# Kernel optimization log

Hardware: AMD Instinct MI355X
Metric: run time of the kernel (lower is better)

Reference implementation:

```python
import jax, jax.numpy as jnp
import numpy as np

B, F, S, D, H = 32, 4096, 8, 512, 2048
N_ITERS = 3
EPS = 1e-8
SCALE = D ** -0.5
LN_EPS = 1e-5  # torch LayerNorm default


def setup_inputs() -> dict:
    key = jax.random.key(0)
    ks = jax.random.split(key, 16)
    w = lambda k, shp: (jax.random.normal(k, shp) * 0.02).astype(jnp.float32)
    d = {
        "slots": jax.random.normal(ks[0], (B, S, D), dtype=jnp.float32),
        "features": jax.random.normal(ks[1], (B, F, D), dtype=jnp.float32),
        # projection weights, stored (in, out) so y = x @ W
        "w_k": w(ks[2], (D, D)),
        "w_v": w(ks[3], (D, D)),
        "w_q": w(ks[4], (D, D)),
        # layer norms
        "ln_feat_w": jnp.ones(D, jnp.float32), "ln_feat_b": jnp.zeros(D, jnp.float32),
        "ln_slot_w": jnp.ones(D, jnp.float32), "ln_slot_b": jnp.zeros(D, jnp.float32),
        # GRUCell (torch layout: gates [r, z, n] stacked on dim0 of [3D, D])
        "gru_w_ih": w(ks[5], (3 * D, D)),
        "gru_w_hh": w(ks[6], (3 * D, D)),
        "gru_b_ih": jnp.zeros(3 * D, jnp.float32),
        "gru_b_hh": jnp.zeros(3 * D, jnp.float32),
        # residual MLP: LN -> Linear(D,H) -> relu -> Linear(H,D)
        "ln_mlp_w": jnp.ones(D, jnp.float32), "ln_mlp_b": jnp.zeros(D, jnp.float32),
        "mlp_w1": w(ks[7], (D, H)), "mlp_b1": jnp.zeros(H, jnp.float32),
        "mlp_w2": w(ks[8], (H, D)), "mlp_b2": jnp.zeros(D, jnp.float32),
    }
    return d


def _ln(x, w, b):
    m = jnp.mean(x, axis=-1, keepdims=True)
    v = jnp.mean(jnp.square(x - m), axis=-1, keepdims=True)
    return (x - m) * jax.lax.rsqrt(v + LN_EPS) * w + b


def _gru_cell(x, h, w_ih, w_hh, b_ih, b_hh):
    # torch.nn.GRUCell semantics; x,h: [..., D]
    gi = x @ w_ih.T + b_ih
    gh = h @ w_hh.T + b_hh
    i_r, i_z, i_n = jnp.split(gi, 3, axis=-1)
    h_r, h_z, h_n = jnp.split(gh, 3, axis=-1)
    r = jax.nn.sigmoid(i_r + h_r)
    z = jax.nn.sigmoid(i_z + h_z)
    n = jnp.tanh(i_n + r * h_n)
    return (1.0 - z) * n + z * h


def reference(slots, features, w_k, w_v, w_q, ln_feat_w, ln_feat_b,
              ln_slot_w, ln_slot_b, gru_w_ih, gru_w_hh, gru_b_ih, gru_b_hh,
              ln_mlp_w, ln_mlp_b, mlp_w1, mlp_b1, mlp_w2, mlp_b2):
    f = _ln(features, ln_feat_w, ln_feat_b)          # [B,F,D]
    keys = f @ w_k                                    # [B,F,D]
    values = f @ w_v                                  # [B,F,D]
    pre_norm_attn = None
    for _ in range(N_ITERS):
        s_n = _ln(slots, ln_slot_w, ln_slot_b)        # [B,S,D]
        q = s_n @ w_q                                 # [B,S,D]
        dots = jnp.einsum('bsd,bfd->bsf', q, keys) * SCALE
        pre_norm_attn = jax.nn.softmax(dots, axis=1)  # softmax over SLOTS
        attn = pre_norm_attn + EPS
        attn = attn / jnp.sum(attn, axis=-1, keepdims=True)
        updates = jnp.einsum('bsf,bfd->bsd', attn, values)
        slots = _gru_cell(updates, s_n, gru_w_ih, gru_w_hh, gru_b_ih, gru_b_hh)
        # residual MLP with initial LayerNorm
        h = _ln(slots, ln_mlp_w, ln_mlp_b)
        h = jax.nn.relu(h @ mlp_w1 + mlp_b1) @ mlp_w2 + mlp_b2
        slots = slots + h
    return slots, pre_norm_attn
```

## Files before the change

kernel.cpp:

```cpp
#include <hip/hip_runtime.h>
#include <hip/hip_bf16.h>
#include <stdint.h>

typedef __hip_bfloat16 bf16;
typedef unsigned short ushort_t;

#define B_ 32
#define F_ 4096
#define S_ 8
#define D_ 512
#define H_ 2048
#define LN_EPS 1e-5f
#define EPS_ 1e-8f
#define SCALE_ 0.044194173824159216f

__device__ __forceinline__ float b2f(ushort_t u){
  union { uint32_t i; float f; } c; c.i = ((uint32_t)u) << 16; return c.f;
}
__device__ __forceinline__ float4 ld4f(const float* p){ return *(const float4*)p; }
__device__ __forceinline__ float4 ld4h(const ushort_t* p){
  ushort4 u = *(const ushort4*)p;
  return make_float4(b2f(u.x), b2f(u.y), b2f(u.z), b2f(u.w));
}
__device__ __forceinline__ float allsum64(float v){
  #pragma unroll
  for (int o = 1; o < 64; o <<= 1) v += __shfl_xor(v, o, 64);
  return v;
}
__device__ __forceinline__ float blockSum256(float v, float* sh){
  v = allsum64(v);
  int wid = threadIdx.x >> 6, lane = threadIdx.x & 63;
  __syncthreads();
  if (lane == 0) sh[wid] = v;
  __syncthreads();
  return sh[0] + sh[1] + sh[2] + sh[3];
}

__global__ void detect_dtype(const uint32_t* __restrict__ w, int* __restrict__ flag){
  __shared__ int sh;
  if (threadIdx.x == 0) sh = 0;
  __syncthreads();
  int c = 0;
  for (int i = threadIdx.x; i < 4096; i += 256){
    uint32_t e = (w[i] >> 7) & 0xFF;
    if (e == 0 || e >= 0xBF) c++;
  }
  atomicAdd(&sh, c);
  __syncthreads();
  if (threadIdx.x == 0) *flag = (sh >= 100) ? 1 : 0;
}

template<int TRANS_B, int BIAS, int RELU, int A_DYN, int B_DYN>
__global__ __launch_bounds__(256) void gemm64(
    const void* __restrict__ A, const void* __restrict__ B,
    const void* __restrict__ bias, float* __restrict__ C,
    int M, int N, int K, int kLen, const int* __restrict__ flag)
{
  const bool f32 = (*flag != 0);
  const bool aF = A_DYN ? f32 : true;
  const bool bF = B_DYN ? f32 : true;
  __shared__ float As[16][68];
  __shared__ float Bs[16][68];
  const int tid = threadIdx.x;
  const int m0 = blockIdx.x * 64, n0 = blockIdx.y * 64;
  const int kBeg = blockIdx.z * kLen;
  const int tm = (tid & 15) * 4, tn = (tid >> 4) * 4;
  const int ar = tid >> 2;
  const int ac = (tid & 3) * 4;
  const int br = tid >> 4;
  const int bc = (tid & 15) * 4;
  float acc[4][4] = {};

  for (int kc = kBeg; kc < kBeg + kLen; kc += 16){
    size_t aidx = (size_t)(m0 + ar) * K + kc + ac;
    float4 a4 = aF ? ld4f((const float*)A + aidx) : ld4h((const ushort_t*)A + aidx);
    As[ac+0][ar] = a4.x; As[ac+1][ar] = a4.y; As[ac+2][ar] = a4.z; As[ac+3][ar] = a4.w;
    if (!TRANS_B){
      size_t bidx = (size_t)(kc + br) * N + n0 + bc;
      float4 b4 = bF ? ld4f((const float*)B + bidx) : ld4h((const ushort_t*)B + bidx);
      Bs[br][bc+0] = b4.x; Bs[br][bc+1] = b4.y; Bs[br][bc+2] = b4.z; Bs[br][bc+3] = b4.w;
    } else {
      size_t bidx = (size_t)(n0 + ar) * K + kc + ac;
      float4 b4 = bF ? ld4f((const float*)B + bidx) : ld4h((const ushort_t*)B + bidx);
      Bs[ac+0][ar] = b4.x; Bs[ac+1][ar] = b4.y; Bs[ac+2][ar] = b4.z; Bs[ac+3][ar] = b4.w;
    }
    __syncthreads();
    #pragma unroll
    for (int k = 0; k < 16; k++){
      float av[4], bv[4];
      #pragma unroll
      for (int i = 0; i < 4; i++) av[i] = As[k][tm + i];
      #pragma unroll
      for (int j = 0; j < 4; j++) bv[j] = Bs[k][tn + j];
      #pragma unroll
      for (int i = 0; i < 4; i++)
        #pragma unroll
        for (int j = 0; j < 4; j++) acc[i][j] += av[i] * bv[j];
    }
    __syncthreads();
  }
  float bb[4] = {0,0,0,0};
  if (BIAS){
    #pragma unroll
    for (int j = 0; j < 4; j++)
      bb[j] = f32 ? ((const float*)bias)[n0 + tn + j]
                  : b2f(((const ushort_t*)bias)[n0 + tn + j]);
  }
  #pragma unroll
  for (int i = 0; i < 4; i++){
    #pragma unroll
    for (int j = 0; j < 4; j++){
      float v = acc[i][j];
      if (BIAS) v += bb[j];
      if (RELU) v = fmaxf(v, 0.0f);
      C[((size_t)blockIdx.z * M + m0 + tm + i) * N + n0 + tn + j] = v;
    }
  }
}

template<int BIAS, int RELU>
__global__ __launch_bounds__(256) void combine4(
    const float* __restrict__ in, const void* __restrict__ bias,
    float* __restrict__ out, int sz, int N)
{
  int i = blockIdx.x * 256 + threadIdx.x;
  float v = in[i] + in[sz + i] + in[2 * sz + i] + in[3 * sz + i];
  if (BIAS) v += b2f(((const ushort_t*)bias)[i % N]);
  if (RELU) v = fmaxf(v, 0.0f);
  out[i] = v;
}

template<int F32>
__global__ __launch_bounds__(256, 2) void big_pass(
    const void* __restrict__ features, const float* __restrict__ qk,
    const void* __restrict__ lnw, const void* __restrict__ lnb,
    void* __restrict__ d_out_base, float* __restrict__ Upart,
    float* __restrict__ Rpart, const int* __restrict__ flag)
{
  if ((*flag != 0) != (F32 != 0)) return;
  __shared__ float Ubuf[4][S_ * D_];
  __shared__ float Rbuf[4][S_];
  __shared__ float pbuf[S_][256];
  const int b = blockIdx.y;
  const int tid = threadIdx.x;
  const int wid = tid >> 6, lane = tid & 63;
  const int fblock = blockIdx.x * 256;
  const int f0 = fblock + wid * 64;

  float lw[8], lb[8];
  #pragma unroll
  for (int j = 0; j < 8; j++){
    int d = 8 * lane + j;
    lw[j] = F32 ? ((const float*)lnw)[d] : b2f(((const ushort_t*)lnw)[d]);
    lb[j] = F32 ? ((const float*)lnb)[d] : b2f(((const ushort_t*)lnb)[d]);
  }
  float qkr[8][8];
  #pragma unroll
  for (int s = 0; s < 8; s++){
    const float* qp = qk + (size_t)(b * S_ + s) * D_ + 8 * lane;
    float4 q0 = *(const float4*)qp;
    float4 q1 = *(const float4*)(qp + 4);
    qkr[s][0]=q0.x; qkr[s][1]=q0.y; qkr[s][2]=q0.z; qkr[s][3]=q0.w;
    qkr[s][4]=q1.x; qkr[s][5]=q1.y; qkr[s][6]=q1.z; qkr[s][7]=q1.w;
  }
  float U[8][8];
  #pragma unroll
  for (int s = 0; s < 8; s++)
    #pragma unroll
    for (int j = 0; j < 8; j++) U[s][j] = 0.0f;
  float racc[8] = {0,0,0,0,0,0,0,0};

  const size_t base = ((size_t)b * F_ + f0) * D_ + 8 * lane;
  const float* fbf = (const float*)features + base;
  const ushort_t* fbh = (const ushort_t*)features + base;
  float4 nf0 = {}, nf1 = {}; uint4 nh = {};
  if (F32){ nf0 = *(const float4*)fbf; nf1 = *(const float4*)(fbf + 4); }
  else    { nh  = *(const uint4*)fbh; }

  for (int r = 0; r < 64; r++){
    float x[8];
    if (F32){
      float4 c0 = nf0, c1 = nf1;
      if (r < 63){
        nf0 = *(const float4*)(fbf + (size_t)(r + 1) * D_);
        nf1 = *(const float4*)(fbf + (size_t)(r + 1) * D_ + 4);
      }
      x[0]=c0.x; x[1]=c0.y; x[2]=c0.z; x[3]=c0.w;
      x[4]=c1.x; x[5]=c1.y; x[6]=c1.z; x[7]=c1.w;
    } else {
      uint4 cx = nh;
      if (r < 63) nh = *(const uint4*)(fbh + (size_t)(r + 1) * D_);
      x[0]=b2f(cx.x & 0xffff); x[1]=b2f(cx.x >> 16);
      x[2]=b2f(cx.y & 0xffff); x[3]=b2f(cx.y >> 16);
      x[4]=b2f(cx.z & 0xffff); x[5]=b2f(cx.z >> 16);
      x[6]=b2f(cx.w & 0xffff); x[7]=b2f(cx.w >> 16);
    }
    float sum = 0.0f;
    #pragma unroll
    for (int j = 0; j < 8; j++) sum += x[j];
    float mean = allsum64(sum) * (1.0f / 512.0f);
    float var = 0.0f;
    #pragma unroll
    for (int j = 0; j < 8; j++){ x[j] -= mean; var += x[j] * x[j]; }
    var = allsum64(var) * (1.0f / 512.0f);
    float rstd = 1.0f / sqrtf(var + LN_EPS);
    float y[8];
    #pragma unroll
    for (int j = 0; j < 8; j++) y[j] = x[j] * rstd * lw[j] + lb[j];

    float dt[8];
    #pragma unroll
    for (int s = 0; s < 8; s++){
      float t = 0.0f;
      #pragma unroll
      for (int j = 0; j < 8; j++) t += qkr[s][j] * y[j];
      dt[s] = allsum64(t) * SCALE_;
    }
    float mx = dt[0];
    #pragma unroll
    for (int s = 1; s < 8; s++) mx = fmaxf(mx, dt[s]);
    float p[8]; float den = 0.0f;
    #pragma unroll
    for (int s = 0; s < 8; s++){ p[s] = __expf(dt[s] - mx); den += p[s]; }
    float inv = 1.0f / den;
    #pragma unroll
    for (int s = 0; s < 8; s++) p[s] *= inv;
    #pragma unroll
    for (int s = 0; s < 8; s++) if (lane == s) pbuf[s][wid * 64 + r] = p[s];
    #pragma unroll
    for (int s = 0; s < 8; s++){
      float pe = p[s] + EPS_;
      racc[s] += pe;
      #pragma unroll
      for (int j = 0; j < 8; j++) U[s][j] += pe * y[j];
    }
  }
  #pragma unroll
  for (int s = 0; s < 8; s++){
    float* ub = &Ubuf[wid][s * D_ + 8 * lane];
    *(float4*)ub     = make_float4(U[s][0], U[s][1], U[s][2], U[s][3]);
    *(float4*)(ub+4) = make_float4(U[s][4], U[s][5], U[s][6], U[s][7]);
  }
  #pragma unroll
  for (int s = 0; s < 8; s++) if (lane == s) Rbuf[wid][s] = racc[s];
  __syncthreads();
  float* up = Upart + (size_t)(b * 16 + blockIdx.x) * S_ * D_;
  for (int e = tid; e < S_ * D_; e += 256)
    up[e] = Ubuf[0][e] + Ubuf[1][e] + Ubuf[2][e] + Ubuf[3][e];
  if (tid < 8)
    Rpart[(b * 16 + blockIdx.x) * S_ + tid] =
        Rbuf[0][tid] + Rbuf[1][tid] + Rbuf[2][tid] + Rbuf[3][tid];
  #pragma unroll
  for (int s = 0; s < 8; s++){
    size_t oi = 131072 + ((size_t)(b * S_ + s)) * F_ + fblock + tid;
    float pv = pbuf[s][tid];
    if (F32) ((float*)d_out_base)[oi] = pv;
    else     ((bf16*)d_out_base)[oi] = __float2bfloat16(pv);
  }
}

__global__ __launch_bounds__(256) void reduce_updates(
    const float* __restrict__ Upart, const float* __restrict__ Rpart,
    float* __restrict__ Ud)
{
  __shared__ float rinv;
  int bs = blockIdx.x;
  int b = bs >> 3, s = bs & 7;
  int t = threadIdx.x;
  if (t == 0){
    float r = 0.0f;
    for (int w = 0; w < 16; w++) r += Rpart[(b * 16 + w) * S_ + s];
    rinv = 1.0f / r;
  }
  __syncthreads();
  const float* up = Upart + ((size_t)(b * 16) * S_ + s) * D_;
  float ri = rinv;
  #pragma unroll
  for (int u = 0; u < 2; u++){
    int e = t + u * 256;
    float acc = 0.0f;
    for (int w = 0; w < 16; w++) acc += up[(size_t)w * S_ * D_ + e];
    Ud[((size_t)(b * S_ + s)) * D_ + e] = acc * ri;
  }
}

__global__ __launch_bounds__(256) void ln_rows(
    const float* __restrict__ x, const void* __restrict__ w,
    const void* __restrict__ b, float* __restrict__ y, const int* __restrict__ flag)
{
  const bool f32 = (*flag != 0);
  __shared__ float sh[4];
  int row = blockIdx.x, t = threadIdx.x;
  const float* xr = x + (size_t)row * D_;
  float v0 = xr[t], v1 = xr[t + 256];
  float mean = blockSum256(v0 + v1, sh) * (1.0f / 512.0f);
  float d0 = v0 - mean, d1 = v1 - mean;
  float var = blockSum256(d0 * d0 + d1 * d1, sh) * (1.0f / 512.0f);
  float rstd = 1.0f / sqrtf(var + LN_EPS);
  float w0 = f32 ? ((const float*)w)[t]       : b2f(((const ushort_t*)w)[t]);
  float w1 = f32 ? ((const float*)w)[t + 256] : b2f(((const ushort_t*)w)[t + 256]);
  float b0 = f32 ? ((const float*)b)[t]       : b2f(((const ushort_t*)b)[t]);
  float b1 = f32 ? ((const float*)b)[t + 256] : b2f(((const ushort_t*)b)[t + 256]);
  y[(size_t)row * D_ + t]       = d0 * rstd * w0 + b0;
  y[(size_t)row * D_ + t + 256] = d1 * rstd * w1 + b1;
}

__global__ __launch_bounds__(256) void gru_gate_ln(
    const float* __restrict__ gi, const float* __restrict__ gh,
    const float* __restrict__ sn, const void* __restrict__ lw,
    const void* __restrict__ lb, float* __restrict__ snew,
    float* __restrict__ lnm, const int* __restrict__ flag)
{
  const bool f32 = (*flag != 0);
  __shared__ float sh[4];
  int row = blockIdx.x, t = threadIdx.x;
  const float* gir = gi + (size_t)row * 1536;
  const float* ghr = gh + (size_t)row * 1536;
  const float* snr = sn + (size_t)row * D_;
  float v[2];
  #pragma unroll
  for (int u = 0; u < 2; u++){
    int d = t + u * 256;
    float ir = gir[d], iz = gir[512 + d], in_ = gir[1024 + d];
    float hr = ghr[d], hz = ghr[512 + d], hn = ghr[1024 + d];
    float rg = 1.0f / (1.0f + __expf(-(ir + hr)));
    float zg = 1.0f / (1.0f + __expf(-(iz + hz)));
    float a  = in_ + rg * hn;
    float e2 = __expf(2.0f * a);
    float ng = 1.0f - 2.0f / (e2 + 1.0f);
    float h  = snr[d];
    v[u] = (1.0f - zg) * ng + zg * h;
    snew[(size_t)row * D_ + d] = v[u];
  }
  float mean = blockSum256(v[0] + v[1], sh) * (1.0f / 512.0f);
  float d0 = v[0] - mean, d1 = v[1] - mean;
  float var = blockSum256(d0 * d0 + d1 * d1, sh) * (1.0f / 512.0f);
  float rstd = 1.0f / sqrtf(var + LN_EPS);
  float w0 = f32 ? ((const float*)lw)[t]       : b2f(((const ushort_t*)lw)[t]);
  float w1 = f32 ? ((const float*)lw)[t + 256] : b2f(((const ushort_t*)lw)[t + 256]);
  float b0 = f32 ? ((const float*)lb)[t]       : b2f(((const ushort_t*)lb)[t]);
  float b1 = f32 ? ((const float*)lb)[t + 256] : b2f(((const ushort_t*)lb)[t + 256]);
  lnm[(size_t)row * D_ + t]       = d0 * rstd * w0 + b0;
  lnm[(size_t)row * D_ + t + 256] = d1 * rstd * w1 + b1;
}

__global__ __launch_bounds__(256) void combine_h2(
    const float* __restrict__ snew, const float* __restrict__ h2p,
    const void* __restrict__ b2, float* __restrict__ slots,
    const int* __restrict__ flag)
{
  const bool f32 = (*flag != 0);
  int idx = blockIdx.x * 256 + threadIdx.x;
  int d = idx & 511;
  float bias = f32 ? ((const float*)b2)[d] : b2f(((const ushort_t*)b2)[d]);
  slots[idx] = snew[idx] + h2p[idx] + h2p[131072 + idx] + h2p[262144 + idx]
             + h2p[393216 + idx] + bias;
}

__global__ __launch_bounds__(256) void cast_in(const void* __restrict__ in,
                                               float* __restrict__ out,
                                               const int* __restrict__ flag){
  const bool f32 = (*flag != 0);
  int i = blockIdx.x * 256 + threadIdx.x;
  out[i] = f32 ? ((const float*)in)[i] : b2f(((const ushort_t*)in)[i]);
}
__global__ __launch_bounds__(256) void store_out(const float* __restrict__ in,
                                                 void* __restrict__ out,
                                                 const int* __restrict__ flag){
  const bool f32 = (*flag != 0);
  int i = blockIdx.x * 256 + threadIdx.x;
  float v = in[i];
  if (f32) ((float*)out)[i] = v;
  else     ((bf16*)out)[i] = __float2bfloat16(v);
}

extern "C" void kernel_launch(void* const* d_in, const int* in_sizes, int n_in,
                              void* d_out, int out_size, void* d_ws, size_t ws_size,
                              hipStream_t stream)
{
  const void* in_slots  = d_in[0];
  const void* features  = d_in[1];
  const void* w_k   = d_in[2];
  const void* w_v   = d_in[3];
  const void* w_q   = d_in[4];
  const void* ln_feat_w = d_in[5];
  const void* ln_feat_b = d_in[6];
  const void* ln_slot_w = d_in[7];
  const void* ln_slot_b = d_in[8];
  const void* w_ih  = d_in[9];
  const void* w_hh  = d_in[10];
  const void* b_ih  = d_in[11];
  const void* b_hh  = d_in[12];
  const void* ln_mlp_w = d_in[13];
  const void* ln_mlp_b = d_in[14];
  const void* mlp_w1 = d_in[15];
  const void* mlp_b1 = d_in[16];
  const void* mlp_w2 = d_in[17];
  const void* mlp_b2 = d_in[18];

  float* W     = (float*)d_ws;
  int*   flag  = (int*)d_ws;
  float* Wqk   = W + 64;
  float* slots = Wqk + 262144;
  float* s_n   = slots + 131072;
  float* qkb   = s_n + 131072;
  float* Ud    = qkb + 131072;
  float* upd   = Ud + 131072;
  float* Rpart = upd + 131072;
  float* P     = Rpart + 4096;
  float* Upart = P;
  float* gi    = P;
  float* gh    = P + 393216;
  float* lnm   = P + 786432;
  float* snew  = P + 917504;
  float* h1    = P + 1048576;
  float* h2p   = P + 1572864;
  float* Wqkp  = P + 2097152;
  float* qkp   = Wqkp + 1048576;
  float* updp  = qkp + 524288;
  float* gip   = updp + 524288;
  float* ghp   = gip + 1572864;
  float* h1p   = ghp + 1572864;

  detect_dtype<<<1, 256, 0, stream>>>((const uint32_t*)features, flag);
  cast_in<<<512, 256, 0, stream>>>(in_slots, slots, flag);
  gemm64<1, 0, 0, 1, 1><<<dim3(8, 8, 4), 256, 0, stream>>>(
      w_q, w_k, nullptr, Wqkp, 512, 512, 512, 128, flag);
  combine4<0, 0><<<1024, 256, 0, stream>>>(Wqkp, nullptr, Wqk, 262144, 512);

  for (int it = 0; it < 3; ++it){
    ln_rows<<<256, 256, 0, stream>>>(slots, ln_slot_w, ln_slot_b, s_n, flag);
    gemm64<0, 0, 0, 0, 0><<<dim3(4, 8, 4), 256, 0, stream>>>(
        s_n, Wqk, nullptr, qkp, 256, 512, 512, 128, flag);
    combine4<0, 0><<<512, 256, 0, stream>>>(qkp, nullptr, qkb, 131072, 512);
    big_pass<0><<<dim3(16, 32), 256, 0, stream>>>(
        features, qkb, ln_feat_w, ln_feat_b, d_out, Upart, Rpart, flag);
    big_pass<1><<<dim3(16, 32), 256, 0, stream>>>(
        features, qkb, ln_feat_w, ln_feat_b, d_out, Upart, Rpart, flag);
    reduce_updates<<<256, 256, 0, stream>>>(Upart, Rpart, Ud);
    gemm64<0, 0, 0, 0, 1><<<dim3(4, 8, 4), 256, 0, stream>>>(
        Ud, w_v, nullptr, updp, 256, 512, 512, 128, flag);
    combine4<0, 0><<<512, 256, 0, stream>>>(updp, nullptr, upd, 131072, 512);
    gemm64<1, 0, 0, 0, 1><<<dim3(4, 24, 4), 256, 0, stream>>>(
        upd, w_ih, nullptr, gip, 256, 1536, 512, 128, flag);
    combine4<1, 0><<<1536, 256, 0, stream>>>(gip, b_ih, gi, 393216, 1536);
    gemm64<1, 0, 0, 0, 1><<<dim3(4, 24, 4), 256, 0, stream>>>(
        s_n, w_hh, nullptr, ghp, 256, 1536, 512, 128, flag);
    combine4<1, 0><<<1536, 256, 0, stream>>>(ghp, b_hh, gh, 393216, 1536);
    gru_gate_ln<<<256, 256, 0, stream>>>(gi, gh, s_n, ln_mlp_w, ln_mlp_b,
                                         snew, lnm, flag);
    gemm64<0, 0, 0, 0, 1><<<dim3(4, 32, 4), 256, 0, stream>>>(
        lnm, mlp_w1, nullptr, h1p, 256, 2048, 512, 128, flag);
    combine4<1, 1><<<2048, 256, 0, stream>>>(h1p, mlp_b1, h1, 524288, 2048);
    gemm64<0, 0, 0, 0, 1><<<dim3(4, 8, 4), 256, 0, stream>>>(
        h1, mlp_w2, nullptr, h2p, 256, 512, 2048, 512, flag);
    combine_h2<<<512, 256, 0, stream>>>(snew, h2p, mlp_b2, slots, flag);
  }
  store_out<<<512, 256, 0, stream>>>(slots, d_out, flag);
}
```

Baseline: 1.096 ms.

## Fuse split-K combines into consumers and precompute W_v·W_ihᵀ product

Removes most combine4 passes by summing split-K partials inside the consuming kernels (big_pass, gru_combine, the second MLP GEMM's A-load with bias and ReLU). It precomputes W_v @ W_ihᵀ once so the value projection and the input-gate GEMM become one GEMM, and merges the gi and gh GEMMs into a single launch. It also drops the duplicate big_pass dtype launch and folds store_out into the last combine. This cuts launch count and intermediate traffic, but the second MLP GEMM now reads four partials plus bias for every A tile load, and reassociating the value matmul changes rounding slightly.

New measurement: 1.187 ms. +8.3%, slower.

```diff
diff --git a/kernel.cpp b/kernel.cpp
--- a/kernel.cpp
+++ b/kernel.cpp
@@ -35,6 +35,9 @@
   __syncthreads();
   return sh[0] + sh[1] + sh[2] + sh[3];
 }
+__device__ __forceinline__ float dynld(const void* p, int i, bool f32){
+  return f32 ? ((const float*)p)[i] : b2f(((const ushort_t*)p)[i]);
+}
 
 __global__ void detect_dtype(const uint32_t* __restrict__ w, int* __restrict__ flag){
   __shared__ int sh;
@@ -50,11 +53,11 @@
   if (threadIdx.x == 0) *flag = (sh >= 100) ? 1 : 0;
 }
 
-template<int TRANS_B, int BIAS, int RELU, int A_DYN, int B_DYN>
+template<int TRANS_B, int A_DYN, int B_DYN, int A_CMB>
 __global__ __launch_bounds__(256) void gemm64(
     const void* __restrict__ A, const void* __restrict__ B,
-    const void* __restrict__ bias, float* __restrict__ C,
-    int M, int N, int K, int kLen, const int* __restrict__ flag)
+    const void* __restrict__ Abias, float* __restrict__ C,
+    int M, int N, int K, int kLen, size_t aPart, const int* __restrict__ flag)
 {
   const bool f32 = (*flag != 0);
   const bool aF = A_DYN ? f32 : true;
@@ -73,7 +76,24 @@
 
   for (int kc = kBeg; kc < kBeg + kLen; kc += 16){
     size_t aidx = (size_t)(m0 + ar) * K + kc + ac;
-    float4 a4 = aF ? ld4f((const float*)A + aidx) : ld4h((const ushort_t*)A + aidx);
+    float4 a4;
+    if (A_CMB){
+      const float* Af = (const float*)A;
+      float4 s0 = ld4f(Af + aidx);
+      float4 s1 = ld4f(Af + aPart + aidx);
+      float4 s2 = ld4f(Af + 2 * aPart + aidx);
+      float4 s3 = ld4f(Af + 3 * aPart + aidx);
+      float bx0 = dynld(Abias, kc + ac + 0, f32);
+      float bx1 = dynld(Abias, kc + ac + 1, f32);
+      float bx2 = dynld(Abias, kc + ac + 2, f32);
+      float bx3 = dynld(Abias, kc + ac + 3, f32);
+      a4.x = fmaxf(s0.x + s1.x + s2.x + s3.x + bx0, 0.0f);
+      a4.y = fmaxf(s0.y + s1.y + s2.y + s3.y + bx1, 0.0f);
+      a4.z = fmaxf(s0.z + s1.z + s2.z + s3.z + bx2, 0.0f);
+      a4.w = fmaxf(s0.w + s1.w + s2.w + s3.w + bx3, 0.0f);
+    } else {
+      a4 = aF ? ld4f((const float*)A + aidx) : ld4h((const ushort_t*)A + aidx);
+    }
     As[ac+0][ar] = a4.x; As[ac+1][ar] = a4.y; As[ac+2][ar] = a4.z; As[ac+3][ar] = a4.w;
     if (!TRANS_B){
       size_t bidx = (size_t)(kc + br) * N + n0 + bc;
@@ -99,45 +119,84 @@
     }
     __syncthreads();
   }
-  float bb[4] = {0,0,0,0};
-  if (BIAS){
+  #pragma unroll
+  for (int i = 0; i < 4; i++)
     #pragma unroll
     for (int j = 0; j < 4; j++)
-      bb[j] = f32 ? ((const float*)bias)[n0 + tn + j]
-                  : b2f(((const ushort_t*)bias)[n0 + tn + j]);
-  }
-  #pragma unroll
-  for (int i = 0; i < 4; i++){
-    #pragma unroll
-    for (int j = 0; j < 4; j++){
-      float v = acc[i][j];
-      if (BIAS) v += bb[j];
-      if (RELU) v = fmaxf(v, 0.0f);
-      C[((size_t)blockIdx.z * M + m0 + tm + i) * N + n0 + tn + j] = v;
-    }
-  }
-}
-
-template<int BIAS, int RELU>
+      C[((size_t)blockIdx.z * M + m0 + tm + i) * N + n0 + tn + j] = acc[i][j];
+}
+
 __global__ __launch_bounds__(256) void combine4(
-    const float* __restrict__ in, const void* __restrict__ bias,
-    float* __restrict__ out, int sz, int N)
+    const float* __restrict__ in, float* __restrict__ out, int sz)
 {
   int i = blockIdx.x * 256 + threadIdx.x;
-  float v = in[i] + in[sz + i] + in[2 * sz + i] + in[3 * sz + i];
-  if (BIAS) v += b2f(((const ushort_t*)bias)[i % N]);
-  if (RELU) v = fmaxf(v, 0.0f);
-  out[i] = v;
-}
-
-template<int F32>
+  out[i] = in[i] + in[sz + i] + in[2 * sz + i] + in[3 * sz + i];
+}
+
+__global__ __launch_bounds__(256) void gemm_gigh(
+    const float* __restrict__ Ud, const float* __restrict__ Wvih,
+    const float* __restrict__ s_n, const void* __restrict__ w_hh,
+    float* __restrict__ gip, float* __restrict__ ghp,
+    const int* __restrict__ flag)
+{
+  const bool f32 = (*flag != 0);
+  const bool doGh = blockIdx.z >= 4;
+  const int kz = blockIdx.z & 3;
+  __shared__ float As[16][68];
+  __shared__ float Bs[16][68];
+  const int tid = threadIdx.x;
+  const int m0 = blockIdx.x * 64, n0 = blockIdx.y * 64;
+  const int kBeg = kz * 128;
+  const int tm = (tid & 15) * 4, tn = (tid >> 4) * 4;
+  const int ar = tid >> 2;
+  const int ac = (tid & 3) * 4;
+  const int br = tid >> 4;
+  const int bc = (tid & 15) * 4;
+  const float* A = doGh ? s_n : Ud;
+  float acc[4][4] = {};
+
+  for (int kc = kBeg; kc < kBeg + 128; kc += 16){
+    float4 a4 = ld4f(A + (size_t)(m0 + ar) * 512 + kc + ac);
+    As[ac+0][ar] = a4.x; As[ac+1][ar] = a4.y; As[ac+2][ar] = a4.z; As[ac+3][ar] = a4.w;
+    if (!doGh){
+      float4 b4 = ld4f(Wvih + (size_t)(kc + br) * 1536 + n0 + bc);
+      Bs[br][bc+0] = b4.x; Bs[br][bc+1] = b4.y; Bs[br][bc+2] = b4.z; Bs[br][bc+3] = b4.w;
+    } else {
+      size_t bidx = (size_t)(n0 + ar) * 512 + kc + ac;
+      float4 b4 = f32 ? ld4f((const float*)w_hh + bidx)
+                      : ld4h((const ushort_t*)w_hh + bidx);
+      Bs[ac+0][ar] = b4.x; Bs[ac+1][ar] = b4.y; Bs[ac+2][ar] = b4.z; Bs[ac+3][ar] = b4.w;
+    }
+    __syncthreads();
+    #pragma unroll
+    for (int k = 0; k < 16; k++){
+      float av[4], bv[4];
+      #pragma unroll
+      for (int i = 0; i < 4; i++) av[i] = As[k][tm + i];
+      #pragma unroll
+      for (int j = 0; j < 4; j++) bv[j] = Bs[k][tn + j];
+      #pragma unroll
+      for (int i = 0; i < 4; i++)
+        #pragma unroll
+        for (int j = 0; j < 4; j++) acc[i][j] += av[i] * bv[j];
+    }
+    __syncthreads();
+  }
+  float* C = (doGh ? ghp : gip) + (size_t)kz * 256 * 1536;
+  #pragma unroll
+  for (int i = 0; i < 4; i++)
+    #pragma unroll
+    for (int j = 0; j < 4; j++)
+      C[(size_t)(m0 + tm + i) * 1536 + n0 + tn + j] = acc[i][j];
+}
+
 __global__ __launch_bounds__(256, 2) void big_pass(
-    const void* __restrict__ features, const float* __restrict__ qk,
+    const void* __restrict__ features, const float* __restrict__ qkp,
     const void* __restrict__ lnw, const void* __restrict__ lnb,
     void* __restrict__ d_out_base, float* __restrict__ Upart,
     float* __restrict__ Rpart, const int* __restrict__ flag)
 {
-  if ((*flag != 0) != (F32 != 0)) return;
+  const bool F32 = (*flag != 0);
   __shared__ float Ubuf[4][S_ * D_];
   __shared__ float Rbuf[4][S_];
   __shared__ float pbuf[S_][256];
@@ -151,15 +210,22 @@
   #pragma unroll
   for (int j = 0; j < 8; j++){
     int d = 8 * lane + j;
-    lw[j] = F32 ? ((const float*)lnw)[d] : b2f(((const ushort_t*)lnw)[d]);
-    lb[j] = F32 ? ((const float*)lnb)[d] : b2f(((const ushort_t*)lnb)[d]);
+    lw[j] = dynld(lnw, d, F32);
+    lb[j] = dynld(lnb, d, F32);
   }
   float qkr[8][8];
   #pragma unroll
   for (int s = 0; s < 8; s++){
-    const float* qp = qk + (size_t)(b * S_ + s) * D_ + 8 * lane;
-    float4 q0 = *(const float4*)qp;
-    float4 q1 = *(const float4*)(qp + 4);
+    const float* qp = qkp + (size_t)(b * S_ + s) * D_ + 8 * lane;
+    float4 q0 = ld4f(qp);
+    float4 q1 = ld4f(qp + 4);
+    #pragma unroll
+    for (int p = 1; p < 4; p++){
+      const float* qq = qp + (size_t)p * 131072;
+      float4 t0 = ld4f(qq), t1 = ld4f(qq + 4);
+      q0.x += t0.x; q0.y += t0.y; q0.z += t0.z; q0.w += t0.w;
+      q1.x += t1.x; q1.y += t1.y; q1.z += t1.z; q1.w += t1.w;
+    }
     qkr[s][0]=q0.x; qkr[s][1]=q0.y; qkr[s][2]=q0.z; qkr[s][3]=q0.w;
     qkr[s][4]=q1.x; qkr[s][5]=q1.y; qkr[s][6]=q1.z; qkr[s][7]=q1.w;
   }
@@ -297,16 +363,15 @@
   float d0 = v0 - mean, d1 = v1 - mean;
   float var = blockSum256(d0 * d0 + d1 * d1, sh) * (1.0f / 512.0f);
   float rstd = 1.0f / sqrtf(var + LN_EPS);
-  float w0 = f32 ? ((const float*)w)[t]       : b2f(((const ushort_t*)w)[t]);
-  float w1 = f32 ? ((const float*)w)[t + 256] : b2f(((const ushort_t*)w)[t + 256]);
-  float b0 = f32 ? ((const float*)b)[t]       : b2f(((const ushort_t*)b)[t]);
-  float b1 = f32 ? ((const float*)b)[t + 256] : b2f(((const ushort_t*)b)[t + 256]);
+  float w0 = dynld(w, t, f32),       w1 = dynld(w, t + 256, f32);
+  float b0 = dynld(b, t, f32),       b1 = dynld(b, t + 256, f32);
   y[(size_t)row * D_ + t]       = d0 * rstd * w0 + b0;
   y[(size_t)row * D_ + t + 256] = d1 * rstd * w1 + b1;
 }
 
-__global__ __launch_bounds__(256) void gru_gate_ln(
-    const float* __restrict__ gi, const float* __restrict__ gh,
+__global__ __launch_bounds__(256) void gru_combine(
+    const float* __restrict__ gip, const float* __restrict__ ghp,
+    const void* __restrict__ b_ih, const void* __restrict__ b_hh,
     const float* __restrict__ sn, const void* __restrict__ lw,
     const void* __restrict__ lb, float* __restrict__ snew,
     float* __restrict__ lnm, const int* __restrict__ flag)
@@ -314,15 +379,25 @@
   const bool f32 = (*flag != 0);
   __shared__ float sh[4];
   int row = blockIdx.x, t = threadIdx.x;
-  const float* gir = gi + (size_t)row * 1536;
-  const float* ghr = gh + (size_t)row * 1536;
   const float* snr = sn + (size_t)row * D_;
   float v[2];
   #pragma unroll
   for (int u = 0; u < 2; u++){
     int d = t + u * 256;
-    float ir = gir[d], iz = gir[512 + d], in_ = gir[1024 + d];
-    float hr = ghr[d], hz = ghr[512 + d], hn = ghr[1024 + d];
+    float ir = 0, iz = 0, in_ = 0, hr = 0, hz = 0, hn = 0;
+    #pragma unroll
+    for (int p = 0; p < 4; p++){
+      const float* gp = gip + (size_t)p * 393216 + (size_t)row * 1536;
+      const float* hp = ghp + (size_t)p * 393216 + (size_t)row * 1536;
+      ir  += gp[d]; iz += gp[512 + d]; in_ += gp[1024 + d];
+      hr  += hp[d]; hz += hp[512 + d]; hn  += hp[1024 + d];
+    }
+    ir  += dynld(b_ih, d, f32);
+    iz  += dynld(b_ih, 512 + d, f32);
+    in_ += dynld(b_ih, 1024 + d, f32);
+    hr  += dynld(b_hh, d, f32);
+    hz  += dynld(b_hh, 512 + d, f32);
+    hn  += dynld(b_hh, 1024 + d, f32);
     float rg = 1.0f / (1.0f + __expf(-(ir + hr)));
     float zg = 1.0f / (1.0f + __expf(-(iz + hz)));
     float a  = in_ + rg * hn;
@@ -336,25 +411,29 @@
   float d0 = v[0] - mean, d1 = v[1] - mean;
   float var = blockSum256(d0 * d0 + d1 * d1, sh) * (1.0f / 512.0f);
   float rstd = 1.0f / sqrtf(var + LN_EPS);
-  float w0 = f32 ? ((const float*)lw)[t]       : b2f(((const ushort_t*)lw)[t]);
-  float w1 = f32 ? ((const float*)lw)[t + 256] : b2f(((const ushort_t*)lw)[t + 256]);
-  float b0 = f32 ? ((const float*)lb)[t]       : b2f(((const ushort_t*)lb)[t]);
-  float b1 = f32 ? ((const float*)lb)[t + 256] : b2f(((const ushort_t*)lb)[t + 256]);
+  float w0 = dynld(lw, t, f32),       w1 = dynld(lw, t + 256, f32);
+  float b0 = dynld(lb, t, f32),       b1 = dynld(lb, t + 256, f32);
   lnm[(size_t)row * D_ + t]       = d0 * rstd * w0 + b0;
   lnm[(size_t)row * D_ + t + 256] = d1 * rstd * w1 + b1;
 }
 
+template<int FINAL>
 __global__ __launch_bounds__(256) void combine_h2(
     const float* __restrict__ snew, const float* __restrict__ h2p,
     const void* __restrict__ b2, float* __restrict__ slots,
-    const int* __restrict__ flag)
+    void* __restrict__ out, const int* __restrict__ flag)
 {
   const bool f32 = (*flag != 0);
   int idx = blockIdx.x * 256 + threadIdx.x;
   int d = idx & 511;
-  float bias = f32 ? ((const float*)b2)[d] : b2f(((const ushort_t*)b2)[d]);
-  slots[idx] = snew[idx] + h2p[idx] + h2p[131072 + idx] + h2p[262144 + idx]
-             + h2p[393216 + idx] + bias;
+  float bias = dynld(b2, d, f32);
+  float v = snew[idx] + h2p[idx] + h2p[131072 + idx] + h2p[262144 + idx]
+          + h2p[393216 + idx] + bias;
+  slots[idx] = v;
+  if (FINAL){
+    if (f32) ((float*)out)[idx] = v;
+    else     ((bf16*)out)[idx] = __float2bfloat16(v);
+  }
 }
 
 __global__ __launch_bounds__(256) void cast_in(const void* __restrict__ in,
@@ -363,15 +442,6 @@
   const bool f32 = (*flag != 0);
   int i = blockIdx.x * 256 + threadIdx.x;
   out[i] = f32 ? ((const float*)in)[i] : b2f(((const ushort_t*)in)[i]);
-}
-__global__ __launch_bounds__(256) void store_out(const float* __restrict__ in,
-                                                 void* __restrict__ out,
-                                                 const int* __restrict__ flag){
-  const bool f32 = (*flag != 0);
-  int i = blockIdx.x * 256 + threadIdx.x;
-  float v = in[i];
-  if (f32) ((float*)out)[i] = v;
-  else     ((bf16*)out)[i] = __float2bfloat16(v);
 }
 
 extern "C" void kernel_launch(void* const* d_in, const int* in_sizes, int n_in,
@@ -401,60 +471,47 @@
   float* W     = (float*)d_ws;
   int*   flag  = (int*)d_ws;
   float* Wqk   = W + 64;
-  float* slots = Wqk + 262144;
+  float* slots = Wqk   + 262144;
   float* s_n   = slots + 131072;
-  float* qkb   = s_n + 131072;
-  float* Ud    = qkb + 131072;
-  float* upd   = Ud + 131072;
-  float* Rpart = upd + 131072;
-  float* P     = Rpart + 4096;
-  float* Upart = P;
-  float* gi    = P;
-  float* gh    = P + 393216;
-  float* lnm   = P + 786432;
-  float* snew  = P + 917504;
-  float* h1    = P + 1048576;
-  float* h2p   = P + 1572864;
-  float* Wqkp  = P + 2097152;
-  float* qkp   = Wqkp + 1048576;
-  float* updp  = qkp + 524288;
-  float* gip   = updp + 524288;
-  float* ghp   = gip + 1572864;
-  float* h1p   = ghp + 1572864;
+  float* qkp   = s_n   + 131072;
+  float* Ud    = qkp   + 524288;
+  float* Rpart = Ud    + 131072;
+  float* Upart = Rpart + 4096;
+  float* gip   = Upart + 2097152;
+  float* ghp   = gip   + 1572864;
+  float* lnm   = ghp   + 1572864;
+  float* snew  = lnm   + 131072;
+  float* h1p   = snew  + 131072;
+  float* h2p   = h1p   + 2097152;
+  float* Wqkp  = h2p   + 524288;
+  float* Wvih  = Wqkp  + 1048576;
 
   detect_dtype<<<1, 256, 0, stream>>>((const uint32_t*)features, flag);
   cast_in<<<512, 256, 0, stream>>>(in_slots, slots, flag);
-  gemm64<1, 0, 0, 1, 1><<<dim3(8, 8, 4), 256, 0, stream>>>(
-      w_q, w_k, nullptr, Wqkp, 512, 512, 512, 128, flag);
-  combine4<0, 0><<<1024, 256, 0, stream>>>(Wqkp, nullptr, Wqk, 262144, 512);
+  gemm64<1, 1, 1, 0><<<dim3(8, 8, 4), 256, 0, stream>>>(
+      w_q, w_k, nullptr, Wqkp, 512, 512, 512, 128, 0, flag);
+  combine4<<<1024, 256, 0, stream>>>(Wqkp, Wqk, 262144);
+  gemm64<1, 1, 1, 0><<<dim3(8, 24, 1), 256, 0, stream>>>(
+      w_v, w_ih, nullptr, Wvih, 512, 1536, 512, 512, 0, flag);
 
   for (int it = 0; it < 3; ++it){
     ln_rows<<<256, 256, 0, stream>>>(slots, ln_slot_w, ln_slot_b, s_n, flag);
-    gemm64<0, 0, 0, 0, 0><<<dim3(4, 8, 4), 256, 0, stream>>>(
-        s_n, Wqk, nullptr, qkp, 256, 512, 512, 128, flag);
-    combine4<0, 0><<<512, 256, 0, stream>>>(qkp, nullptr, qkb, 131072, 512);
-    big_pass<0><<<dim3(16, 32), 256, 0, stream>>>(
-        features, qkb, ln_feat_w, ln_feat_b, d_out, Upart, Rpart, flag);
-    big_pass<1><<<dim3(16, 32), 256, 0, stream>>>(
-        features, qkb, ln_feat_w, ln_feat_b, d_out, Upart, Rpart, flag);
+    gemm64<0, 0, 0, 0><<<dim3(4, 8, 4), 256, 0, stream>>>(
+        s_n, Wqk, nullptr, qkp, 256, 512, 512, 128, 0, flag);
+    big_pass<<<dim3(16, 32), 256, 0, stream>>>(
+        features, qkp, ln_feat_w, ln_feat_b, d_out, Upart, Rpart, flag);
     reduce_updates<<<256, 256, 0, stream>>>(Upart, Rpart, Ud);
-    gemm64<0, 0, 0, 0, 1><<<dim3(4, 8, 4), 256, 0, stream>>>(
-        Ud, w_v, nullptr, updp, 256, 512, 512, 128, flag);
-    combine4<0, 0><<<512, 256, 0, stream>>>(updp, nullptr, upd, 131072, 512);
-    gemm64<1, 0, 0, 0, 1><<<dim3(4, 24, 4), 256, 0, stream>>>(
-        upd, w_ih, nullptr, gip, 256, 1536, 512, 128, flag);
-    combine4<1, 0><<<1536, 256, 0, stream>>>(gip, b_ih, gi, 393216, 1536);
-    gemm64<1, 0, 0, 0, 1><<<dim3(4, 24, 4), 256, 0, stream>>>(
-        s_n, w_hh, nullptr, ghp, 256, 1536, 512, 128, flag);
-    combine4<1, 0><<<1536, 256, 0, stream>>>(ghp, b_hh, gh, 393216, 1536);
-    gru_gate_ln<<<256, 256, 0, stream>>>(gi, gh, s_n, ln_mlp_w, ln_mlp_b,
-                                         snew, lnm, flag);
-    gemm64<0, 0, 0, 0, 1><<<dim3(4, 32, 4), 256, 0, stream>>>(
-        lnm, mlp_w1, nullptr, h1p, 256, 2048, 512, 128, flag);
-    combine4<1, 1><<<2048, 256, 0, stream>>>(h1p, mlp_b1, h1, 524288, 2048);
-    gemm64<0, 0, 0, 0, 1><<<dim3(4, 8, 4), 256, 0, stream>>>(
-        h1, mlp_w2, nullptr, h2p, 256, 512, 2048, 512, flag);
-    combine_h2<<<512, 256, 0, stream>>>(snew, h2p, mlp_b2, slots, flag);
-  }
-  store_out<<<512, 256, 0, stream>>>(slots, d_out, flag);
-}
+    gemm_gigh<<<dim3(4, 24, 8), 256, 0, stream>>>(
+        Ud, Wvih, s_n, w_hh, gip, ghp, flag);
+    gru_combine<<<256, 256, 0, stream>>>(gip, ghp, b_ih, b_hh, s_n,
+                                         ln_mlp_w, ln_mlp_b, snew, lnm, flag);
+    gemm64<0, 0, 1, 0><<<dim3(4, 32, 4), 256, 0, stream>>>(
+        lnm, mlp_w1, nullptr, h1p, 256, 2048, 512, 128, 0, flag);
+    gemm64<0, 0, 1, 1><<<dim3(4, 8, 4), 256, 0, stream>>>(
+        h1p, mlp_w2, mlp_b1, h2p, 256, 512, 2048, 512, 524288, flag);
+    if (it < 2)
+      combine_h2<0><<<512, 256, 0, stream>>>(snew, h2p, mlp_b2, slots, d_out, flag);
+    else
+      combine_h2<1><<<512, 256, 0, stream>>>(snew, h2p, mlp_b2, slots, d_out, flag);
+  }
+}
```
